# Performance work log

Measured on AMD Instinct MI355X. Metric: run time of the kernel, lower is better.

Reference implementation:

```python
import jax, jax.numpy as jnp
import numpy as np

B, N, D = 4, 1024, 1024
H = 16
RS, RC = 32, 32
MLP = int(D * 4.0)
EPS = 1e-6


def _ln(x):
    # LayerNorm with no scale/bias (flax defaults: eps=1e-6)
    m = jnp.mean(x, axis=-1, keepdims=True)
    v = jnp.mean(jnp.square(x - m), axis=-1, keepdims=True)
    return (x - m) * jax.lax.rsqrt(v + EPS)


def _rms(x, scale):
    rms = jnp.sqrt(jnp.mean(jnp.square(x), axis=-1, keepdims=True) + EPS)
    return scale * x / rms


def _modulate(x, shift, scale):
    return x * (1 + scale[:, None]) + shift[:, None]


def setup_inputs() -> dict:
    key = jax.random.key(0)
    ks = jax.random.split(key, 20)
    s = 0.02
    return {
        'x': jax.random.normal(ks[0], (B, N, D), jnp.float32),
        'c': jax.random.normal(ks[1], (B, D), jnp.float32),
        'cls_token': jax.random.normal(ks[2], (B, D), jnp.float32),
        'Wc': jax.random.normal(ks[3], (D, 6 * D), jnp.float32) * s,
        'bc': jax.random.normal(ks[4], (6 * D,), jnp.float32) * s,
        'Wqkv': jax.random.normal(ks[5], (D, 3 * D), jnp.float32) * s,
        'bqkv': jnp.zeros((3 * D,), jnp.float32),
        'Wo': jax.random.normal(ks[6], (D, D), jnp.float32) * s,
        'bo': jnp.zeros((D,), jnp.float32),
        'A_s': jax.random.normal(ks[7], (D, RS), jnp.float32) * s,
        'B_s': jax.random.normal(ks[8], (RS, D), jnp.float32) * s,
        'rms_s_scale': jnp.ones((D,), jnp.float32),
        'C_r': jax.random.normal(ks[9], (D, RC), jnp.float32) * s,
        'D_r': jax.random.normal(ks[10], (RC, D), jnp.float32) * s,
        'rms_c_scale': jnp.ones((D,), jnp.float32),
        'W1': jax.random.normal(ks[11], (D, MLP), jnp.float32) * s,
        'b1': jnp.zeros((MLP,), jnp.float32),
        'W2': jax.random.normal(ks[12], (MLP, D), jnp.float32) * s,
        'b2': jnp.zeros((D,), jnp.float32),
    }


def reference(x, c, cls_token, Wc, bc, Wqkv, bqkv, Wo, bo, A_s, B_s,
              rms_s_scale, C_r, D_r, rms_c_scale, W1, b1, W2, b2):
    hd = D // H
    # AdaLN conditioning
    c_proj = jax.nn.silu(c) @ Wc + bc                    # (B, 6D)
    shift_a, scale_a, gate_a, shift_m, scale_m, gate_m = jnp.split(c_proj, 6, axis=-1)

    # Self-attention branch
    x_norm = _modulate(_ln(x), shift_a, scale_a)         # (B, N, D)
    qkv = x_norm @ Wqkv + bqkv                           # (B, N, 3D)
    q, k, v = jnp.split(qkv, 3, axis=-1)
    q = q.reshape(B, N, H, hd).transpose(0, 2, 1, 3)     # (B, H, N, hd)
    k = k.reshape(B, N, H, hd).transpose(0, 2, 1, 3)
    v = v.reshape(B, N, H, hd).transpose(0, 2, 1, 3)
    attn_w = jax.nn.softmax(jnp.einsum('bhqd,bhkd->bhqk', q, k) * hd ** (-0.5), axis=-1)
    attn_out = jnp.einsum('bhqk,bhkd->bhqd', attn_w, v)
    attn_out = attn_out.transpose(0, 2, 1, 3).reshape(B, N, D)
    attn_out = attn_out @ Wo + bo
    Y = x + gate_a[:, None] * attn_out

    # Self-gram low-rank branch (residual)
    gram_s = (x @ A_s) @ B_s                             # (B, N, D)
    X_prime = _rms(gram_s, rms_s_scale) + Y

    # Cross-gram branch via CLS token (no residual)
    u_c = cls_token[:, :, None] * C_r[None]              # (B, D, RC)
    v_c = jnp.einsum('bnd,bdr->bnr', X_prime, u_c)       # (B, N, RC)
    gram_c = v_c @ D_r                                   # (B, N, D)
    Z = _rms(gram_c, rms_c_scale)

    # MLP branch
    z_norm = _modulate(_ln(Z), shift_m, scale_m)
    h = jax.nn.gelu(z_norm @ W1 + b1) @ W2 + b2
    return Z + gate_m[:, None] * h
```

## Files before the change

### kernel.cpp

```cpp
#include <hip/hip_runtime.h>
#include <stdint.h>

typedef float  f32x4  __attribute__((ext_vector_type(4)));
typedef short  s16x8  __attribute__((ext_vector_type(8)));
typedef __bf16 bf16x4 __attribute__((ext_vector_type(4)));

#define D_    1024
#define SIXD  6144
#define QSCALE 0.18033688011112042f

#define BAR() asm volatile("s_barrier" ::: "memory")

__device__ __forceinline__ f32x4 mfma_b(const s16x8 &a, const s16x8 &b, const f32x4 &c) {
  return __builtin_amdgcn_mfma_f32_16x16x32_bf16(a, b, c, 0, 0, 0);
}

__device__ __forceinline__ void gload_lds16(const void* g, void* l) {
  __builtin_amdgcn_global_load_lds(
      (const __attribute__((address_space(1))) uint32_t*)g,
      (__attribute__((address_space(3))) uint32_t*)l, 16, 0, 0);
}

__global__ __launch_bounds__(256)
void prep(const float* __restrict__ c, const float* __restrict__ Wc,
          const float* __restrict__ bc, float* __restrict__ cproj,
          const float* __restrict__ Wqkv, const float* __restrict__ Wo,
          const float* __restrict__ W1, const float* __restrict__ W2,
          __bf16* __restrict__ Wqkvt, __bf16* __restrict__ Wot,
          __bf16* __restrict__ W1t, __bf16* __restrict__ W2t)
{
  __shared__ float sc[4096];
  __shared__ float tp[8][4][32];
  __shared__ __bf16 tt[64][65];
  int tid = threadIdx.x;
  if (blockIdx.x < 192) {
    for (int i = tid; i < 4096; i += 256) {
      float v = c[i];
      sc[i] = v / (1.f + __expf(-v));
    }
    __syncthreads();
    int colo = tid & 31, kseg = tid >> 5;
    int col = blockIdx.x * 32 + colo;
    float a0 = 0.f, a1 = 0.f, a2 = 0.f, a3 = 0.f;
    for (int k = kseg * 128; k < kseg * 128 + 128; k++) {
      float w = Wc[(size_t)k * SIXD + col];
      a0 += sc[k] * w; a1 += sc[1024 + k] * w;
      a2 += sc[2048 + k] * w; a3 += sc[3072 + k] * w;
    }
    tp[kseg][0][colo] = a0; tp[kseg][1][colo] = a1;
    tp[kseg][2][colo] = a2; tp[kseg][3][colo] = a3;
    __syncthreads();
    if (kseg == 0) {
#pragma unroll
      for (int b = 0; b < 4; b++) {
        float s = bc[col];
#pragma unroll
        for (int g = 0; g < 8; g++) s += tp[g][b][colo];
        cproj[b * SIXD + col] = s;
      }
    }
    return;
  }
  int bid = blockIdx.x - 192;
  const float* W; __bf16* Wt; int Kdim, Ndim, lb;
  if (bid < 768)       { W = Wqkv; Wt = Wqkvt; Kdim = 1024; Ndim = 3072; lb = bid; }
  else if (bid < 1024) { W = Wo;   Wt = Wot;   Kdim = 1024; Ndim = 1024; lb = bid - 768; }
  else if (bid < 2048) { W = W1;   Wt = W1t;   Kdim = 1024; Ndim = 4096; lb = bid - 1024; }
  else                 { W = W2;   Wt = W2t;   Kdim = 4096; Ndim = 1024; lb = bid - 2048; }
  int ntn = Ndim >> 6;
  int kt = lb / ntn, nt = lb % ntn;
  const float* src = W + (size_t)(kt * 64) * Ndim + nt * 64;
#pragma unroll
  for (int i = 0; i < 4; i++) {
    int k = i * 16 + (tid >> 4);
    int c4 = tid & 15;
    float4 v = ((const float4*)(src + (size_t)k * Ndim))[c4];
    tt[k][c4 * 4 + 0] = (__bf16)v.x; tt[k][c4 * 4 + 1] = (__bf16)v.y;
    tt[k][c4 * 4 + 2] = (__bf16)v.z; tt[k][c4 * 4 + 3] = (__bf16)v.w;
  }
  __syncthreads();
  __bf16* dst = Wt + (size_t)(nt * 64) * Kdim + kt * 64;
  int n = tid >> 2, ks = (tid & 3) * 16;
  bf16x4 o0, o1, o2, o3;
#pragma unroll
  for (int j = 0; j < 4; j++) {
    o0[j] = tt[ks + j][n];      o1[j] = tt[ks + 4 + j][n];
    o2[j] = tt[ks + 8 + j][n];  o3[j] = tt[ks + 12 + j][n];
  }
  __bf16* dp = dst + (size_t)n * Kdim + ks;
  *(bf16x4*)(dp) = o0; *(bf16x4*)(dp + 4) = o1;
  *(bf16x4*)(dp + 8) = o2; *(bf16x4*)(dp + 12) = o3;
}

__global__ __launch_bounds__(256)
void transpose_v(const __bf16* __restrict__ qkv, __bf16* __restrict__ Vt)
{
  __shared__ __bf16 t[32][33];
  int bid = blockIdx.x;
  int dt = bid & 1, nt = (bid >> 1) & 31, bh = bid >> 6;
  int b = bh >> 4, h = bh & 15;
  int x = threadIdx.x & 31, yq = threadIdx.x >> 5;
  const __bf16* src = qkv + ((size_t)(b * 1024 + nt * 32)) * 3072 + 2048 + h * 64 + dt * 32;
#pragma unroll
  for (int i = 0; i < 4; i++) {
    int row = yq * 4 + i;
    t[row][x] = src[(size_t)row * 3072 + x];
  }
  __syncthreads();
  __bf16* dst = Vt + ((size_t)(bh * 64 + dt * 32)) * 1024 + nt * 32;
#pragma unroll
  for (int i = 0; i < 4; i++) {
    int drow = yq * 4 + i;
    dst[(size_t)drow * 1024 + x] = t[x][drow];
  }
}

__global__ __launch_bounds__(256)
void ln_mod(const float* __restrict__ X, const float* __restrict__ cproj,
            int shift_off, int scale_off, __bf16* __restrict__ Out)
{
  int row = blockIdx.x;
  int b = row >> 10;
  int tid = threadIdx.x;
  const float4* xr = (const float4*)(X + (size_t)row * D_);
  float4 v = xr[tid];
  float s  = v.x + v.y + v.z + v.w;
  float s2 = v.x * v.x + v.y * v.y + v.z * v.z + v.w * v.w;
#pragma unroll
  for (int off = 1; off < 64; off <<= 1) {
    s  += __shfl_xor(s,  off, 64);
    s2 += __shfl_xor(s2, off, 64);
  }
  __shared__ float red[8];
  int wave = tid >> 6, lane = tid & 63;
  if (lane == 0) { red[wave] = s; red[4 + wave] = s2; }
  __syncthreads();
  s  = red[0] + red[1] + red[2] + red[3];
  s2 = red[4] + red[5] + red[6] + red[7];
  float mean = s * (1.f / D_);
  float var  = s2 * (1.f / D_) - mean * mean;
  float rstd = rsqrtf(var + 1e-6f);
  const float4* sh = (const float4*)(cproj + b * SIXD + shift_off);
  const float4* sc = (const float4*)(cproj + b * SIXD + scale_off);
  float4 shv = sh[tid], scv = sc[tid];
  bf16x4 o;
  o[0] = (__bf16)((v.x - mean) * rstd * (1.f + scv.x) + shv.x);
  o[1] = (__bf16)((v.y - mean) * rstd * (1.f + scv.y) + shv.y);
  o[2] = (__bf16)((v.z - mean) * rstd * (1.f + scv.z) + shv.z);
  o[3] = (__bf16)((v.w - mean) * rstd * (1.f + scv.w) + shv.w);
  *(bf16x4*)(Out + (size_t)row * D_ + tid * 4) = o;
}

template<int EPI, int NBUF>
__global__ __launch_bounds__(256)
void gemm_bt(const __bf16* __restrict__ A, const __bf16* __restrict__ Bt,
             const float* __restrict__ bias, const float* __restrict__ cproj,
             int gate_off, const float* __restrict__ resid,
             void* __restrict__ Cout, void* __restrict__ Cout2,
             void* __restrict__ Cout3, void* __restrict__ Cout4,
             int M, int N, int K, int SK)
{
  __shared__ __align__(16) __bf16 As[NBUF * 128 * 32];
  __shared__ __align__(16) __bf16 Bs[NBUF * 128 * 32];
  const int PD = NBUF - 1;
  int tilesN = N >> 7, tilesM = M >> 7;
  int npersk = tilesM * tilesN;
  int sk = blockIdx.x / npersk;
  int rest = blockIdx.x % npersk;
  int cpx = npersk >> 3;
  rest = (rest & 7) * cpx + (rest >> 3);
  int bm = rest / tilesN, bn = rest % tilesN;
  int Klen = K / SK, Kstart = sk * Klen;

  int tid = threadIdx.x;
  int lane = tid & 63, wave = tid >> 6;
  int lr = lane & 15, lg = lane >> 4;
  int wm = (wave >> 1) << 6, wn = (wave & 1) << 6;

  f32x4 acc[4][4] = {};

  int sr = tid >> 2, skb = tid & 3;
  int scol = ((skb ^ ((sr >> 1) & 3)) * 8);
  const __bf16* pa = A + (size_t)((bm << 7) + sr) * K + Kstart + scol;
  const __bf16* pb = Bt + (size_t)((bn << 7) + sr) * K + Kstart + scol;
  const size_t rstep = (size_t)64 * K;
  __bf16* la = As + tid * 8;
  __bf16* lb = Bs + tid * 8;

  auto STAGE = [&](int buf, int k0) {
    int bo = buf * 4096;
    gload_lds16(pa + k0, la + bo);
    gload_lds16(pa + rstep + k0, la + bo + 2048);
    gload_lds16(pb + k0, lb + bo);
    gload_lds16(pb + rstep + k0, lb + bo + 2048);
  };

  int nt = Klen >> 5;
#pragma unroll
  for (int p = 0; p < PD; p++) STAGE(p, p * 32);

  for (int t = 0; t < nt; t++) {
    if (t + PD < nt) STAGE((t + PD) % NBUF, (t + PD) * 32);
    int ahead = nt - 1 - t; if (ahead > PD) ahead = PD;
    if (ahead >= 3)      asm volatile("s_waitcnt vmcnt(12)" ::: "memory");
    else if (ahead == 2) asm volatile("s_waitcnt vmcnt(8)" ::: "memory");
    else if (ahead == 1) asm volatile("s_waitcnt vmcnt(4)" ::: "memory");
    else                 asm volatile("s_waitcnt vmcnt(0)" ::: "memory");
    BAR();
    const __bf16* Ac = As + (t % NBUF) * 4096;
    const __bf16* Bc = Bs + (t % NBUF) * 4096;
    s16x8 af[4], bfv[4];
#pragma unroll
    for (int m = 0; m < 4; m++) {
      int row = wm + m * 16 + lr;
      af[m] = *(const s16x8*)(Ac + row * 32 + ((lg ^ ((row >> 1) & 3)) * 8));
    }
#pragma unroll
    for (int n = 0; n < 4; n++) {
      int row = wn + n * 16 + lr;
      bfv[n] = *(const s16x8*)(Bc + row * 32 + ((lg ^ ((row >> 1) & 3)) * 8));
    }
    asm volatile("s_waitcnt lgkmcnt(0)" ::: "memory");
    __builtin_amdgcn_sched_barrier(0);
    BAR();
    __builtin_amdgcn_s_setprio(1);
#pragma unroll
    for (int m = 0; m < 4; m++)
#pragma unroll
      for (int n = 0; n < 4; n++)
        acc[m][n] = mfma_b(af[m], bfv[n], acc[m][n]);
    __builtin_amdgcn_s_setprio(0);
  }
  asm volatile("s_waitcnt vmcnt(0)" ::: "memory");

  __bf16* Pp = nullptr;
  if (EPI == 3) {
    if (sk == 0)      Pp = (__bf16*)Cout;
    else if (sk == 1) Pp = (__bf16*)Cout2;
    else if (sk == 2) Pp = (__bf16*)Cout3;
    else              Pp = (__bf16*)Cout4;
  }

  int row0 = (bm << 7) + wm;
  int col0 = (bn << 7) + wn;
#pragma unroll
  for (int m = 0; m < 4; m++) {
#pragma unroll
    for (int n = 0; n < 4; n++) {
      int cc = col0 + n * 16 + lr;
      float bv = (EPI == 3) ? 0.f : bias[cc];
#pragma unroll
      for (int r = 0; r < 4; r++) {
        int row = row0 + m * 16 + (lg << 2) + r;
        float v = acc[m][n][r] + bv;
        size_t idx = (size_t)row * N + cc;
        if (EPI == 0) {
          ((__bf16*)Cout)[idx] = (__bf16)v;
        } else if (EPI == 1) {
          int b = row >> 10;
          float g = cproj[b * SIXD + gate_off + cc];
          ((float*)Cout)[idx] = resid[idx] + g * v;
        } else if (EPI == 2) {
          float u = 0.7978845608028654f * (v + 0.044715f * v * v * v);
          u = fminf(fmaxf(u, -15.f), 15.f);
          float e = __expf(2.f * u);
          float th = (e - 1.f) / (e + 1.f);
          ((__bf16*)Cout)[idx] = (__bf16)(0.5f * v * (1.f + th));
        } else if (EPI == 4) {
          float scq = (cc < 1024) ? QSCALE : 1.f;
          ((__bf16*)Cout)[idx] = (__bf16)(v * scq);
        } else {
          Pp[idx] = (__bf16)v;
        }
      }
    }
  }
}

template<int EPI, int NT, int KD>
__global__ __launch_bounds__(512, 2)
void gemm256(const __bf16* __restrict__ A, const __bf16* __restrict__ Bt,
             const float* __restrict__ bias,
             void* __restrict__ Cout, void* __restrict__ Cout2,
             void* __restrict__ Cout3, void* __restrict__ Cout4,
             int M, int N)
{
  __shared__ __align__(16) __bf16 As[2 * 16384];
  __shared__ __align__(16) __bf16 Bs[2 * 16384];
  int tilesN = N >> 8, tilesM = M >> 8;
  int npersk = tilesM * tilesN;
  int sk = blockIdx.x / npersk;
  int rest = blockIdx.x % npersk;
  int cpx = npersk >> 3;
  rest = (rest & 7) * cpx + (rest >> 3);
  int bm = rest / tilesN, bn = rest % tilesN;
  int Kstart = sk * (NT * 64);

  int tid = threadIdx.x;
  int lane = tid & 63, wave = tid >> 6;
  int lr = lane & 15, lg = lane >> 4;
  int wr = wave >> 2, wc = wave & 3;

  f32x4 acc[8][4] = {};

  int srow = tid >> 3;
  int schunk = (tid & 7) ^ (srow & 7);
  const __bf16* pa = A  + (size_t)((bm << 8) + srow) * KD + Kstart + schunk * 8;
  const __bf16* pb = Bt + (size_t)((bn << 8) + srow) * KD + Kstart + schunk * 8;
  __bf16* la = As + tid * 8;
  __bf16* lb = Bs + tid * 8;

  auto SAq = [&](int t, int q) {
    gload_lds16(pa + (size_t)(q * 64) * KD + t * 64,
                la + (t & 1) * 16384 + q * 4096);
  };
  auto SBq = [&](int t, int q) {
    gload_lds16(pb + (size_t)(q * 64) * KD + t * 64,
                lb + (t & 1) * 16384 + q * 4096);
  };

#pragma unroll
  for (int q = 0; q < 4; q++) { SAq(0, q); }
#pragma unroll
  for (int q = 0; q < 4; q++) { SBq(0, q); }
#pragma unroll
  for (int q = 0; q < 4; q++) { SAq(1, q); }
#pragma unroll
  for (int q = 0; q < 4; q++) { SBq(1, q); }
  asm volatile("s_waitcnt vmcnt(8)" ::: "memory");
  BAR();

  int cc0 = ((lg ^ (lr & 7)) << 4);
  int cc1 = cc0 ^ 64;
  const char* aA = (const char*)As + (wr * 128 + lr) * 128;
  const char* aB = (const char*)Bs + (wc * 64 + lr) * 128;

  s16x8 alo[4][2], ahi[4][2], b0v[2][2], b1v[2][2];
#pragma unroll
  for (int m = 0; m < 4; m++) {
    alo[m][0] = *(const s16x8*)(aA + m * 2048 + cc0);
    alo[m][1] = *(const s16x8*)(aA + m * 2048 + cc1);
  }
#pragma unroll
  for (int n = 0; n < 2; n++) {
    b0v[n][0] = *(const s16x8*)(aB + n * 2048 + cc0);
    b0v[n][1] = *(const s16x8*)(aB + n * 2048 + cc1);
  }

  for (int t = 0; t < NT; t++) {
    const char* Ab = aA + (t & 1) * 32768;
    const char* Bb = aB + (t & 1) * 32768;

#pragma unroll
    for (int n = 0; n < 2; n++) {
      b1v[n][0] = *(const s16x8*)(Bb + 4096 + n * 2048 + cc0);
      b1v[n][1] = *(const s16x8*)(Bb + 4096 + n * 2048 + cc1);
    }
    __builtin_amdgcn_sched_barrier(0);
    __builtin_amdgcn_s_setprio(1);
#pragma unroll
    for (int m = 0; m < 4; m++)
#pragma unroll
      for (int n = 0; n < 2; n++) {
        acc[m][n] = mfma_b(alo[m][0], b0v[n][0], acc[m][n]);
        acc[m][n] = mfma_b(alo[m][1], b0v[n][1], acc[m][n]);
      }
    __builtin_amdgcn_s_setprio(0);
    asm volatile("s_waitcnt lgkmcnt(0)" ::: "memory");
    BAR();

#pragma unroll
    for (int m = 0; m < 4; m++) {
      ahi[m][0] = *(const s16x8*)(Ab + 8192 + m * 2048 + cc0);
      ahi[m][1] = *(const s16x8*)(Ab + 8192 + m * 2048 + cc1);
    }
    if (t + 2 < NT) { SBq(t + 2, 0); SBq(t + 2, 1); }
    __builtin_amdgcn_sched_barrier(0);
    __builtin_amdgcn_s_setprio(1);
#pragma unroll
    for (int m = 0; m < 4; m++)
#pragma unroll
      for (int n = 0; n < 2; n++) {
        acc[m][2 + n] = mfma_b(alo[m][0], b1v[n][0], acc[m][2 + n]);
        acc[m][2 + n] = mfma_b(alo[m][1], b1v[n][1], acc[m][2 + n]);
      }
    __builtin_amdgcn_s_setprio(0);
    asm volatile("s_waitcnt lgkmcnt(0)" ::: "memory");
    BAR();

    if (t + 2 < NT) {
      SBq(t + 2, 2); SBq(t + 2, 3);
      SAq(t + 2, 0); SAq(t + 2, 1); SAq(t + 2, 2); SAq(t + 2, 3);
    }
    __builtin_amdgcn_sched_barrier(0);
    __builtin_amdgcn_s_setprio(1);
#pragma unroll
    for (int m = 0; m < 4; m++)
#pragma unroll
      for (int n = 0; n < 2; n++) {
        acc[4 + m][2 + n] = mfma_b(ahi[m][0], b1v[n][0], acc[4 + m][2 + n]);
        acc[4 + m][2 + n] = mfma_b(ahi[m][1], b1v[n][1], acc[4 + m][2 + n]);
      }
#pragma unroll
    for (int m = 0; m < 4; m++)
#pragma unroll
      for (int n = 0; n < 2; n++) {
        acc[4 + m][n] = mfma_b(ahi[m][0], b0v[n][0], acc[4 + m][n]);
        acc[4 + m][n] = mfma_b(ahi[m][1], b0v[n][1], acc[4 + m][n]);
      }
    __builtin_amdgcn_s_setprio(0);
    if (t + 1 < NT) {
      if (t + 2 < NT) asm volatile("s_waitcnt vmcnt(8)" ::: "memory");
      else            asm volatile("s_waitcnt vmcnt(0)" ::: "memory");
      BAR();
      const char* An = aA + ((t + 1) & 1) * 32768;
      const char* Bn = aB + ((t + 1) & 1) * 32768;
#pragma unroll
      for (int m = 0; m < 4; m++) {
        alo[m][0] = *(const s16x8*)(An + m * 2048 + cc0);
        alo[m][1] = *(const s16x8*)(An + m * 2048 + cc1);
      }
#pragma unroll
      for (int n = 0; n < 2; n++) {
        b0v[n][0] = *(const s16x8*)(Bn + n * 2048 + cc0);
        b0v[n][1] = *(const s16x8*)(Bn + n * 2048 + cc1);
      }
    }
  }
  asm volatile("s_waitcnt lgkmcnt(0)" ::: "memory");

  __bf16* Pp = nullptr;
  if (EPI == 3) {
    if (sk == 0)      Pp = (__bf16*)Cout;
    else if (sk == 1) Pp = (__bf16*)Cout2;
    else if (sk == 2) Pp = (__bf16*)Cout3;
    else              Pp = (__bf16*)Cout4;
  }

  int row0 = (bm << 8) + wr * 128;
  int col0 = (bn << 8) + wc * 64;
#pragma unroll
  for (int m = 0; m < 8; m++) {
#pragma unroll
    for (int n = 0; n < 4; n++) {
      int cc = col0 + n * 16 + lr;
      float bv = (EPI == 3) ? 0.f : bias[cc];
#pragma unroll
      for (int r = 0; r < 4; r++) {
        int row = row0 + m * 16 + (lg << 2) + r;
        float v = acc[m][n][r] + bv;
        size_t idx = (size_t)row * N + cc;
        if (EPI == 2) {
          float u = 0.7978845608028654f * (v + 0.044715f * v * v * v);
          u = fminf(fmaxf(u, -15.f), 15.f);
          float e = __expf(2.f * u);
          float th = (e - 1.f) / (e + 1.f);
          ((__bf16*)Cout)[idx] = (__bf16)(0.5f * v * (1.f + th));
        } else if (EPI == 4) {
          float scq = (cc < 1024) ? QSCALE : 1.f;
          ((__bf16*)Cout)[idx] = (__bf16)(v * scq);
        } else {
          Pp[idx] = (__bf16)v;
        }
      }
    }
  }
}

__global__ __launch_bounds__(256)
void reduce_w2(const __bf16* __restrict__ P0, const __bf16* __restrict__ P1,
               const __bf16* __restrict__ P2, const __bf16* __restrict__ P3,
               const float* __restrict__ bias, const float* __restrict__ cproj,
               float* __restrict__ Out)
{
  int row = blockIdx.x;
  int b = row >> 10;
  int tid = threadIdx.x;
  size_t base = (size_t)row * D_ + tid * 4;
  bf16x4 a0 = *(const bf16x4*)(P0 + base);
  bf16x4 a1 = *(const bf16x4*)(P1 + base);
  bf16x4 a2 = *(const bf16x4*)(P2 + base);
  bf16x4 a3 = *(const bf16x4*)(P3 + base);
  f32x4 s;
#pragma unroll
  for (int i = 0; i < 4; i++)
    s[i] = ((float)a0[i] + (float)a1[i]) + ((float)a2[i] + (float)a3[i]);
  f32x4 bz = *(const f32x4*)(bias + tid * 4);
  f32x4 g  = *(const f32x4*)(cproj + b * SIXD + 5120 + tid * 4);
  f32x4 z  = *(const f32x4*)(Out + base);
  *(f32x4*)(Out + base) = z + g * (s + bz);
}

__global__ __launch_bounds__(512, 4)
void attn_flash(const __bf16* __restrict__ qkv, const __bf16* __restrict__ Vt,
                __bf16* __restrict__ O)
{
  __shared__ __align__(16) __bf16 Kl[2][64 * 64];
  __shared__ __align__(16) __bf16 Vl[2][64 * 64];
  __shared__ __align__(16) __bf16 Pl[8][16 * 64];

  int bid = ((blockIdx.x & 7) << 6) | (blockIdx.x >> 3);
  int qt = bid & 7, h = (bid >> 3) & 15, b = bid >> 7;
  int tid = threadIdx.x, wave = tid >> 6, lane = tid & 63;
  int lr = lane & 15, lg = lane >> 4;

  size_t tok0 = (size_t)b * 1024;
  int qrow = qt * 128 + wave * 16 + lr;
  const __bf16* qptr = qkv + (tok0 + qrow) * 3072 + h * 64;
  s16x8 qf0 = *(const s16x8*)(qptr + lg * 8);
  s16x8 qf1 = *(const s16x8*)(qptr + 32 + lg * 8);

  float l_acc[4] = {0.f, 0.f, 0.f, 0.f};
  f32x4 oacc[4] = {};

  const __bf16* kbase = qkv + tok0 * 3072 + 1024 + h * 64;
  const __bf16* vbase = Vt + ((size_t)(b * 16 + h) * 64) * 1024;

  int skey = tid >> 3, sdb = tid & 7;
  const __bf16* ksrc = kbase + (size_t)skey * 3072 + ((sdb ^ (skey & 7)) * 8);
  const __bf16* vsrc = vbase + (size_t)skey * 1024 + ((sdb ^ (skey & 7)) * 8);
  __bf16* klp = &Kl[0][0] + tid * 8;
  __bf16* vlp = &Vl[0][0] + tid * 8;
  __bf16* pl = &Pl[wave][0];

  auto STAGE = [&](int buf, int kk) {
    gload_lds16(ksrc + (size_t)kk * 3072, klp + buf * 4096);
    gload_lds16(vsrc + kk, vlp + buf * 4096);
  };

  STAGE(0, 0);
  int cur = 0;
  for (int k0 = 0; k0 < 1024; k0 += 64) {
    int kn = (k0 + 64 < 1024) ? (k0 + 64) : k0;
    STAGE(cur ^ 1, kn);
    asm volatile("s_waitcnt vmcnt(2)" ::: "memory");
    BAR();
    const __bf16* K_ = &Kl[cur][0];
    const __bf16* V_ = &Vl[cur][0];

    f32x4 s[4];
    __builtin_amdgcn_s_setprio(1);
#pragma unroll
    for (int n = 0; n < 4; n++) {
      int key = n * 16 + lr;
      int kx = key & 7;
      s16x8 kf0 = *(const s16x8*)(K_ + key * 64 + ((lg ^ kx) * 8));
      s16x8 kf1 = *(const s16x8*)(K_ + key * 64 + (((4 + lg) ^ kx) * 8));
      f32x4 sa = {0.f, 0.f, 0.f, 0.f};
      sa = mfma_b(qf0, kf0, sa);
      sa = mfma_b(qf1, kf1, sa);
      s[n] = sa;
    }
    __builtin_amdgcn_s_setprio(0);

#pragma unroll
    for (int n = 0; n < 4; n++)
#pragma unroll
      for (int r = 0; r < 4; r++)
        s[n][r] = exp2f(s[n][r]);
#pragma unroll
    for (int r = 0; r < 4; r++)
      l_acc[r] += (s[0][r] + s[1][r]) + (s[2][r] + s[3][r]);

#pragma unroll
    for (int n = 0; n < 4; n++)
#pragma unroll
      for (int r = 0; r < 4; r++) {
        int prow = lg * 4 + r;
        int key = n * 16 + lr;
        int idx = prow * 64 + (((key >> 3) ^ (prow & 7)) * 8) + (key & 7);
        pl[idx] = (__bf16)s[n][r];
      }
    asm volatile("s_waitcnt lgkmcnt(0)" ::: "memory");
    __builtin_amdgcn_sched_barrier(0);
    s16x8 pf0 = *(const s16x8*)(pl + lr * 64 + ((lg ^ (lr & 7)) * 8));
    s16x8 pf1 = *(const s16x8*)(pl + lr * 64 + (((4 + lg) ^ (lr & 7)) * 8));

    __builtin_amdgcn_s_setprio(1);
#pragma unroll
    for (int dt = 0; dt < 4; dt++) {
      int vrow = dt * 16 + lr, rx = vrow & 7;
      s16x8 vf0 = *(const s16x8*)(V_ + vrow * 64 + ((lg ^ rx) * 8));
      s16x8 vf1 = *(const s16x8*)(V_ + vrow * 64 + (((4 + lg) ^ rx) * 8));
      oacc[dt] = mfma_b(pf0, vf0, oacc[dt]);
      oacc[dt] = mfma_b(pf1, vf1, oacc[dt]);
    }
    __builtin_amdgcn_s_setprio(0);
    asm volatile("s_waitcnt lgkmcnt(0)" ::: "memory");
    __builtin_amdgcn_sched_barrier(0);
    BAR();
    cur ^= 1;
  }
  asm volatile("s_waitcnt vmcnt(0)" ::: "memory");

  float rinv[4];
#pragma unroll
  for (int r = 0; r < 4; r++) {
    float v = l_acc[r];
#pragma unroll
    for (int off = 1; off < 16; off <<= 1) v += __shfl_xor(v, off, 64);
    rinv[r] = 1.f / v;
  }

  int orow = qt * 128 + wave * 16 + (lg << 2);
#pragma unroll
  for (int dt = 0; dt < 4; dt++)
#pragma unroll
    for (int r = 0; r < 4; r++) {
      float v = oacc[dt][r] * rinv[r];
      O[(tok0 + orow + r) * 1024 + h * 64 + dt * 16 + lr] = (__bf16)v;
    }
}

__global__ __launch_bounds__(256)
void gram_fused(const float* __restrict__ X, const float* __restrict__ Y,
                const float* __restrict__ cls,
                const float* __restrict__ A_s, const float* __restrict__ B_s,
                const float* __restrict__ rms_s,
                const float* __restrict__ C_r, const float* __restrict__ D_r,
                const float* __restrict__ rms_c,
                const float* __restrict__ cproj,
                float* __restrict__ Z, __bf16* __restrict__ Znorm)
{
  __shared__ float xs[4][D_];
  __shared__ float tp[8][4][32];
  __shared__ float t1[4][32];
  __shared__ float red[4][4];
  __shared__ float red2[4][4][2];
  int row0 = blockIdx.x * 4;
  int b = row0 >> 10;
  int tid = threadIdx.x;
  int wv = tid >> 6;

  f32x4 cv = *(const f32x4*)(cls + (size_t)b * D_ + tid * 4);
  f32x4 yv[4];
#pragma unroll
  for (int rr = 0; rr < 4; rr++) {
    ((f32x4*)xs[rr])[tid] = *(const f32x4*)(X + (size_t)(row0 + rr) * D_ + tid * 4);
    yv[rr] = *(const f32x4*)(Y + (size_t)(row0 + rr) * D_ + tid * 4);
  }
  __syncthreads();

  {
    int r = tid & 31, seg = tid >> 5;
    float a0 = 0.f, a1 = 0.f, a2 = 0.f, a3 = 0.f;
    const float* ap = A_s + r;
    for (int d = seg * 128; d < seg * 128 + 128; d++) {
      float w = ap[d * 32];
      a0 += xs[0][d] * w; a1 += xs[1][d] * w;
      a2 += xs[2][d] * w; a3 += xs[3][d] * w;
    }
    tp[seg][0][r] = a0; tp[seg][1][r] = a1; tp[seg][2][r] = a2; tp[seg][3][r] = a3;
  }
  __syncthreads();
  if (tid < 128) {
    int rr = tid >> 5, r = tid & 31;
    float sv = 0.f;
#pragma unroll
    for (int g = 0; g < 8; g++) sv += tp[g][rr][r];
    t1[rr][r] = sv;
  }
  __syncthreads();

  f32x4 g[4] = {};
  for (int r = 0; r < 32; r++) {
    f32x4 bv = *(const f32x4*)(B_s + (size_t)r * D_ + tid * 4);
    g[0] += t1[0][r] * bv; g[1] += t1[1][r] * bv;
    g[2] += t1[2][r] * bv; g[3] += t1[3][r] * bv;
  }
  float ssl[4];
#pragma unroll
  for (int rr = 0; rr < 4; rr++)
    ssl[rr] = g[rr][0]*g[rr][0] + g[rr][1]*g[rr][1] + g[rr][2]*g[rr][2] + g[rr][3]*g[rr][3];
#pragma unroll
  for (int off = 1; off < 64; off <<= 1)
#pragma unroll
    for (int rr = 0; rr < 4; rr++) ssl[rr] += __shfl_xor(ssl[rr], off, 64);
  if ((tid & 63) == 0) {
#pragma unroll
    for (int rr = 0; rr < 4; rr++) red[wv][rr] = ssl[rr];
  }
  __syncthreads();
  {
    f32x4 scv = *(const f32x4*)(rms_s + tid * 4);
#pragma unroll
    for (int rr = 0; rr < 4; rr++) {
      float ss = red[0][rr] + red[1][rr] + red[2][rr] + red[3][rr];
      float rs = rsqrtf(ss * (1.f / D_) + 1e-6f);
      f32x4 xp = scv * g[rr] * rs + yv[rr];
      ((f32x4*)xs[rr])[tid] = xp * cv;
    }
  }
  __syncthreads();

  {
    int r = tid & 31, seg = tid >> 5;
    float a0 = 0.f, a1 = 0.f, a2 = 0.f, a3 = 0.f;
    const float* cp = C_r + r;
    for (int d = seg * 128; d < seg * 128 + 128; d++) {
      float w = cp[d * 32];
      a0 += xs[0][d] * w; a1 += xs[1][d] * w;
      a2 += xs[2][d] * w; a3 += xs[3][d] * w;
    }
    tp[seg][0][r] = a0; tp[seg][1][r] = a1; tp[seg][2][r] = a2; tp[seg][3][r] = a3;
  }
  __syncthreads();
  if (tid < 128) {
    int rr = tid >> 5, r = tid & 31;
    float sv = 0.f;
#pragma unroll
    for (int g2i = 0; g2i < 8; g2i++) sv += tp[g2i][rr][r];
    t1[rr][r] = sv;
  }
  __syncthreads();

  f32x4 g2[4] = {};
  for (int r = 0; r < 32; r++) {
    f32x4 bv = *(const f32x4*)(D_r + (size_t)r * D_ + tid * 4);
    g2[0] += t1[0][r] * bv; g2[1] += t1[1][r] * bv;
    g2[2] += t1[2][r] * bv; g2[3] += t1[3][r] * bv;
  }
#pragma unroll
  for (int rr = 0; rr < 4; rr++)
    ssl[rr] = g2[rr][0]*g2[rr][0] + g2[rr][1]*g2[rr][1] + g2[rr][2]*g2[rr][2] + g2[rr][3]*g2[rr][3];
#pragma unroll
  for (int off = 1; off < 64; off <<= 1)
#pragma unroll
    for (int rr = 0; rr < 4; rr++) ssl[rr] += __shfl_xor(ssl[rr], off, 64);
  if ((tid & 63) == 0) {
#pragma unroll
    for (int rr = 0; rr < 4; rr++) red[wv][rr] = ssl[rr];
  }
  __syncthreads();
  f32x4 z[4];
  {
    f32x4 scv = *(const f32x4*)(rms_c + tid * 4);
#pragma unroll
    for (int rr = 0; rr < 4; rr++) {
      float ss = red[0][rr] + red[1][rr] + red[2][rr] + red[3][rr];
      float rs = rsqrtf(ss * (1.f / D_) + 1e-6f);
      z[rr] = scv * g2[rr] * rs;
    }
  }

  float s1l[4], s2l[4];
#pragma unroll
  for (int rr = 0; rr < 4; rr++) {
    s1l[rr] = z[rr][0] + z[rr][1] + z[rr][2] + z[rr][3];
    s2l[rr] = z[rr][0]*z[rr][0] + z[rr][1]*z[rr][1] + z[rr][2]*z[rr][2] + z[rr][3]*z[rr][3];
  }
#pragma unroll
  for (int off = 1; off < 64; off <<= 1)
#pragma unroll
    for (int rr = 0; rr < 4; rr++) {
      s1l[rr] += __shfl_xor(s1l[rr], off, 64);
      s2l[rr] += __shfl_xor(s2l[rr], off, 64);
    }
  if ((tid & 63) == 0) {
#pragma unroll
    for (int rr = 0; rr < 4; rr++) { red2[wv][rr][0] = s1l[rr]; red2[wv][rr][1] = s2l[rr]; }
  }
  __syncthreads();
  f32x4 shv = *(const f32x4*)(cproj + b * SIXD + 3072 + tid * 4);
  f32x4 scm = *(const f32x4*)(cproj + b * SIXD + 4096 + tid * 4);
#pragma unroll
  for (int rr = 0; rr < 4; rr++) {
    float S  = red2[0][rr][0] + red2[1][rr][0] + red2[2][rr][0] + red2[3][rr][0];
    float S2 = red2[0][rr][1] + red2[1][rr][1] + red2[2][rr][1] + red2[3][rr][1];
    float mean = S * (1.f / D_);
    float var  = S2 * (1.f / D_) - mean * mean;
    float rstd = rsqrtf(var + 1e-6f);
    f32x4 zn = (z[rr] - mean) * rstd * (scm + 1.f) + shv;
    *(f32x4*)(Z + (size_t)(row0 + rr) * D_ + tid * 4) = z[rr];
    bf16x4 o;
#pragma unroll
    for (int i = 0; i < 4; i++) o[i] = (__bf16)zn[i];
    *(bf16x4*)(Znorm + (size_t)(row0 + rr) * D_ + tid * 4) = o;
  }
}

extern "C" void kernel_launch(void* const* d_in, const int* in_sizes, int n_in,
                              void* d_out, int out_size, void* d_ws, size_t ws_size,
                              hipStream_t stream)
{
  const float* x     = (const float*)d_in[0];
  const float* c     = (const float*)d_in[1];
  const float* cls   = (const float*)d_in[2];
  const float* Wc    = (const float*)d_in[3];
  const float* bc    = (const float*)d_in[4];
  const float* Wqkv  = (const float*)d_in[5];
  const float* bqkv  = (const float*)d_in[6];
  const float* Wo    = (const float*)d_in[7];
  const float* bo    = (const float*)d_in[8];
  const float* A_s   = (const float*)d_in[9];
  const float* B_s   = (const float*)d_in[10];
  const float* rms_s = (const float*)d_in[11];
  const float* C_r   = (const float*)d_in[12];
  const float* D_r   = (const float*)d_in[13];
  const float* rms_c = (const float*)d_in[14];
  const float* W1    = (const float*)d_in[15];
  const float* b1    = (const float*)d_in[16];
  const float* W2    = (const float*)d_in[17];
  const float* b2    = (const float*)d_in[18];
  float* out = (float*)d_out;

  float* ws = (float*)d_ws;
  __bf16* Wqkvt = (__bf16*)(ws + 0);
  __bf16* Wot   = (__bf16*)(ws + 1572864);
  __bf16* W1t   = (__bf16*)(ws + 2097152);
  __bf16* W2t   = (__bf16*)(ws + 4194304);
  float*  cproj = ws + 6291456;
  __bf16* xnorm = (__bf16*)(ws + 6316032);
  __bf16* qkv   = (__bf16*)(ws + 8413184);
  __bf16* Vt    = (__bf16*)(ws + 14704640);
  __bf16* h1    = (__bf16*)(ws + 8413184);
  __bf16* attno = (__bf16*)(ws + 16801792);
  float*  Ybuf  = ws + 18898944;
  __bf16* P0 = (__bf16*)(ws + 0);
  __bf16* P1 = (__bf16*)(ws + 2097152);
  __bf16* P2 = (__bf16*)(ws + 16801792);
  __bf16* P3 = (__bf16*)(ws + 18898944);

  prep<<<3264, 256, 0, stream>>>(c, Wc, bc, cproj,
                                 Wqkv, Wo, W1, W2, Wqkvt, Wot, W1t, W2t);
  ln_mod<<<4096, 256, 0, stream>>>(x, cproj, 0, 1024, xnorm);
  gemm256<4, 16, 1024><<<192, 512, 0, stream>>>(xnorm, Wqkvt, bqkv,
                                                qkv, nullptr, nullptr, nullptr,
                                                4096, 3072);
  transpose_v<<<4096, 256, 0, stream>>>(qkv, Vt);
  attn_flash<<<512, 512, 0, stream>>>(qkv, Vt, attno);
  gemm_bt<1, 4><<<256, 256, 0, stream>>>(attno, Wot, bo, cproj, 2048, x,
                                         Ybuf, nullptr, nullptr, nullptr,
                                         4096, 1024, 1024, 1);
  gram_fused<<<1024, 256, 0, stream>>>(x, Ybuf, cls, A_s, B_s, rms_s,
                                       C_r, D_r, rms_c, cproj, out, xnorm);
  gemm256<2, 16, 1024><<<256, 512, 0, stream>>>(xnorm, W1t, b1,
                                                h1, nullptr, nullptr, nullptr,
                                                4096, 4096);
  gemm256<3, 16, 4096><<<256, 512, 0, stream>>>(h1, W2t, nullptr,
                                                P0, P1, P2, P3, 4096, 1024);
  reduce_w2<<<4096, 256, 0, stream>>>(P0, P1, P2, P3, b2, cproj, out);
}
```

Before: 256.5 us.

## Fuse V transpose into QKV GEMM epilogue and widen weight-prep transpose tiles

The QKV GEMM epilogue now writes the V columns straight into the transposed Vt layout as 4-token bf16 vectors, so the separate transpose_v kernel and its extra read and write of V are gone. The weight-conversion part of prep now handles a 256x64 tile per block instead of 64x64, cutting the grid from 3264 to 960 blocks and writing 16-byte vectors. In exchange, the V stores from the epilogue are strided by 1024 elements, and prep uses more shared memory per block, which may lower occupancy.

```diff
diff --git a/kernel.cpp b/kernel.cpp
--- a/kernel.cpp
+++ b/kernel.cpp
@@ -4,6 +4,7 @@
 typedef float  f32x4  __attribute__((ext_vector_type(4)));
 typedef short  s16x8  __attribute__((ext_vector_type(8)));
 typedef __bf16 bf16x4 __attribute__((ext_vector_type(4)));
+typedef __bf16 bf16x8 __attribute__((ext_vector_type(8)));
 
 #define D_    1024
 #define SIXD  6144
@@ -29,11 +30,11 @@
           __bf16* __restrict__ Wqkvt, __bf16* __restrict__ Wot,
           __bf16* __restrict__ W1t, __bf16* __restrict__ W2t)
 {
-  __shared__ float sc[4096];
-  __shared__ float tp[8][4][32];
-  __shared__ __bf16 tt[64][65];
+  __shared__ __align__(16) char smem[33280];
   int tid = threadIdx.x;
   if (blockIdx.x < 192) {
+    float* sc = (float*)smem;
+    float (*tp)[4][32] = (float(*)[4][32])(smem + 16384);
     for (int i = tid; i < 4096; i += 256) {
       float v = c[i];
       sc[i] = v / (1.f + __expf(-v));
@@ -63,55 +64,40 @@
   }
   int bid = blockIdx.x - 192;
   const float* W; __bf16* Wt; int Kdim, Ndim, lb;
-  if (bid < 768)       { W = Wqkv; Wt = Wqkvt; Kdim = 1024; Ndim = 3072; lb = bid; }
-  else if (bid < 1024) { W = Wo;   Wt = Wot;   Kdim = 1024; Ndim = 1024; lb = bid - 768; }
-  else if (bid < 2048) { W = W1;   Wt = W1t;   Kdim = 1024; Ndim = 4096; lb = bid - 1024; }
-  else                 { W = W2;   Wt = W2t;   Kdim = 4096; Ndim = 1024; lb = bid - 2048; }
+  if (bid < 192)      { W = Wqkv; Wt = Wqkvt; Kdim = 1024; Ndim = 3072; lb = bid; }
+  else if (bid < 256) { W = Wo;   Wt = Wot;   Kdim = 1024; Ndim = 1024; lb = bid - 192; }
+  else if (bid < 512) { W = W1;   Wt = W1t;   Kdim = 1024; Ndim = 4096; lb = bid - 256; }
+  else                { W = W2;   Wt = W2t;   Kdim = 4096; Ndim = 1024; lb = bid - 512; }
   int ntn = Ndim >> 6;
-  int kt = lb / ntn, nt = lb % ntn;
-  const float* src = W + (size_t)(kt * 64) * Ndim + nt * 64;
-#pragma unroll
-  for (int i = 0; i < 4; i++) {
-    int k = i * 16 + (tid >> 4);
-    int c4 = tid & 15;
-    float4 v = ((const float4*)(src + (size_t)k * Ndim))[c4];
-    tt[k][c4 * 4 + 0] = (__bf16)v.x; tt[k][c4 * 4 + 1] = (__bf16)v.y;
-    tt[k][c4 * 4 + 2] = (__bf16)v.z; tt[k][c4 * 4 + 3] = (__bf16)v.w;
-  }
-  __syncthreads();
-  __bf16* dst = Wt + (size_t)(nt * 64) * Kdim + kt * 64;
+  int ktg = lb / ntn, nt = lb % ntn;
+  __bf16* tt = (__bf16*)smem;
+  const float* src = W + (size_t)(ktg * 256) * Ndim + nt * 64;
+  int krow = tid >> 4, c4 = tid & 15;
+#pragma unroll
+  for (int t = 0; t < 4; t++) {
+#pragma unroll
+    for (int i = 0; i < 4; i++) {
+      int k = i * 16 + krow;
+      float4 v = ((const float4*)(src + (size_t)(t * 64 + k) * Ndim))[c4];
+      __bf16* row = tt + (t * 64 + k) * 65 + c4 * 4;
+      row[0] = (__bf16)v.x; row[1] = (__bf16)v.y;
+      row[2] = (__bf16)v.z; row[3] = (__bf16)v.w;
+    }
+  }
+  __syncthreads();
+  __bf16* dst = Wt + (size_t)(nt * 64) * Kdim + ktg * 256;
   int n = tid >> 2, ks = (tid & 3) * 16;
-  bf16x4 o0, o1, o2, o3;
-#pragma unroll
-  for (int j = 0; j < 4; j++) {
-    o0[j] = tt[ks + j][n];      o1[j] = tt[ks + 4 + j][n];
-    o2[j] = tt[ks + 8 + j][n];  o3[j] = tt[ks + 12 + j][n];
-  }
-  __bf16* dp = dst + (size_t)n * Kdim + ks;
-  *(bf16x4*)(dp) = o0; *(bf16x4*)(dp + 4) = o1;
-  *(bf16x4*)(dp + 8) = o2; *(bf16x4*)(dp + 12) = o3;
-}
-
-__global__ __launch_bounds__(256)
-void transpose_v(const __bf16* __restrict__ qkv, __bf16* __restrict__ Vt)
-{
-  __shared__ __bf16 t[32][33];
-  int bid = blockIdx.x;
-  int dt = bid & 1, nt = (bid >> 1) & 31, bh = bid >> 6;
-  int b = bh >> 4, h = bh & 15;
-  int x = threadIdx.x & 31, yq = threadIdx.x >> 5;
-  const __bf16* src = qkv + ((size_t)(b * 1024 + nt * 32)) * 3072 + 2048 + h * 64 + dt * 32;
-#pragma unroll
-  for (int i = 0; i < 4; i++) {
-    int row = yq * 4 + i;
-    t[row][x] = src[(size_t)row * 3072 + x];
-  }
-  __syncthreads();
-  __bf16* dst = Vt + ((size_t)(bh * 64 + dt * 32)) * 1024 + nt * 32;
-#pragma unroll
-  for (int i = 0; i < 4; i++) {
-    int drow = yq * 4 + i;
-    dst[(size_t)drow * 1024 + x] = t[x][drow];
+#pragma unroll
+  for (int t = 0; t < 4; t++) {
+    bf16x8 lo, hi;
+#pragma unroll
+    for (int j = 0; j < 8; j++) {
+      lo[j] = tt[(t * 64 + ks + j) * 65 + n];
+      hi[j] = tt[(t * 64 + ks + 8 + j) * 65 + n];
+    }
+    __bf16* dp = dst + (size_t)n * Kdim + t * 64 + ks;
+    *(bf16x8*)(dp) = lo;
+    *(bf16x8*)(dp + 8) = hi;
   }
 }
 
@@ -445,6 +431,16 @@
     for (int n = 0; n < 4; n++) {
       int cc = col0 + n * 16 + lr;
       float bv = (EPI == 3) ? 0.f : bias[cc];
+      if (EPI == 5 && cc >= 2048) {
+        int rbase = row0 + m * 16 + (lg << 2);
+        int dd = cc - 2048;
+        int bb = rbase >> 10, ntok = rbase & 1023;
+        bf16x4 o;
+#pragma unroll
+        for (int r = 0; r < 4; r++) o[r] = (__bf16)(acc[m][n][r] + bv);
+        *(bf16x4*)((__bf16*)Cout2 + ((size_t)(bb << 10) + dd) * 1024 + ntok) = o;
+        continue;
+      }
 #pragma unroll
       for (int r = 0; r < 4; r++) {
         int row = row0 + m * 16 + (lg << 2) + r;
@@ -456,7 +452,7 @@
           float e = __expf(2.f * u);
           float th = (e - 1.f) / (e + 1.f);
           ((__bf16*)Cout)[idx] = (__bf16)(0.5f * v * (1.f + th));
-        } else if (EPI == 4) {
+        } else if (EPI == 5) {
           float scq = (cc < 1024) ? QSCALE : 1.f;
           ((__bf16*)Cout)[idx] = (__bf16)(v * scq);
         } else {
@@ -821,13 +817,12 @@
   __bf16* P2 = (__bf16*)(ws + 16801792);
   __bf16* P3 = (__bf16*)(ws + 18898944);
 
-  prep<<<3264, 256, 0, stream>>>(c, Wc, bc, cproj,
-                                 Wqkv, Wo, W1, W2, Wqkvt, Wot, W1t, W2t);
+  prep<<<960, 256, 0, stream>>>(c, Wc, bc, cproj,
+                                Wqkv, Wo, W1, W2, Wqkvt, Wot, W1t, W2t);
   ln_mod<<<4096, 256, 0, stream>>>(x, cproj, 0, 1024, xnorm);
-  gemm256<4, 16, 1024><<<192, 512, 0, stream>>>(xnorm, Wqkvt, bqkv,
-                                                qkv, nullptr, nullptr, nullptr,
+  gemm256<5, 16, 1024><<<192, 512, 0, stream>>>(xnorm, Wqkvt, bqkv,
+                                                qkv, Vt, nullptr, nullptr,
                                                 4096, 3072);
-  transpose_v<<<4096, 256, 0, stream>>>(qkv, Vt);
   attn_flash<<<512, 512, 0, stream>>>(qkv, Vt, attno);
   gemm_bt<1, 4><<<256, 256, 0, stream>>>(attno, Wot, bo, cproj, 2048, x,
                                          Ybuf, nullptr, nullptr, nullptr,
```

Result: no change. 253.7 us (median of 2 runs) (-1.1%).
